# Kernel optimization log

Measured on AMD Instinct MI355X. Metric: run time of the kernel, lower is better.

The kernel has to match this reference:

```python
import jax, jax.numpy as jnp
import numpy as np

B, S, D, H = 4, 2048, 1024, 16
HD = D // H  # head_dim = 64


def setup_inputs() -> dict:
    key = jax.random.key(0)
    kx, kq, kk, kv, ko = jax.random.split(key, 5)
    scale = 1.0 / np.sqrt(D)
    return {
        "x": jax.random.normal(kx, (B, S, D), dtype=jnp.float32),
        "wq": jax.random.normal(kq, (D, D), dtype=jnp.float32) * scale,
        "wk": jax.random.normal(kk, (D, D), dtype=jnp.float32) * scale,
        "wv": jax.random.normal(kv, (D, D), dtype=jnp.float32) * scale,
        "wo": jax.random.normal(ko, (D, D), dtype=jnp.float32) * scale,
    }


def reference(x, wq, wk, wv, wo):
    b, s, d = x.shape
    # nn.Linear stores weight [out, in]: y = x @ W.T
    q = (x @ wq.T).reshape(b, s, H, HD)
    k = (x @ wk.T).reshape(b, s, H, HD)
    v = (x @ wv.T).reshape(b, s, H, HD)
    # scores: [b, h, s, s]
    scores = jnp.einsum("bqhd,bkhd->bhqk", q, k) / np.sqrt(HD)
    causal = jnp.triu(jnp.ones((s, s), dtype=bool), k=1)
    scores = jnp.where(causal, -jnp.inf, scores)
    attn = jax.nn.softmax(scores, axis=-1)
    out = jnp.einsum("bhqk,bkhd->bqhd", attn, v).reshape(b, s, d)
    return out @ wo.T
```

## Files before the change

kernel.cpp:

```cpp
#include <hip/hip_runtime.h>
#include <math.h>

typedef unsigned short u16;
typedef __attribute__((ext_vector_type(8))) short short8;
typedef __attribute__((ext_vector_type(4))) short short4v;
typedef __attribute__((ext_vector_type(4))) float f32x4;

constexpr int Bn = 4, Sn = 2048, Dn = 1024, Hn = 16;
constexpr float SCL = 0.125f * 1.44269504f;

__device__ __forceinline__ u16 f2bf(float f) {
  unsigned u = __float_as_uint(f);
  u += 0x7fffu + ((u >> 16) & 1u);
  return (u16)(u >> 16);
}
__device__ __forceinline__ u16 f2bf_t(float f) {
  return (u16)(__float_as_uint(f) >> 16);
}

__device__ __forceinline__ f32x4 mfma32(short8 a, short8 b, f32x4 c) {
  return __builtin_amdgcn_mfma_f32_16x16x32_bf16(a, b, c, 0, 0, 0);
}

__device__ __forceinline__ f32x4 mfma16(short4v a, short4v b, f32x4 c) {
#if __has_builtin(__builtin_amdgcn_mfma_f32_16x16x16_bf16)
  return __builtin_amdgcn_mfma_f32_16x16x16_bf16(a, b, c, 0, 0, 0);
#elif __has_builtin(__builtin_amdgcn_mfma_f32_16x16x16bf16_1k)
  return __builtin_amdgcn_mfma_f32_16x16x16bf16_1k(a, b, c, 0, 0, 0);
#else
  short8 a8 = {a[0], a[1], a[2], a[3], 0, 0, 0, 0};
  short8 b8 = {b[0], b[1], b[2], b[3], 0, 0, 0, 0};
  return __builtin_amdgcn_mfma_f32_16x16x32_bf16(a8, b8, c, 0, 0, 0);
#endif
}

__device__ __forceinline__ void gl_lds16(const u16* g, u16* l) {
  __builtin_amdgcn_global_load_lds(
      (const __attribute__((address_space(1))) unsigned int*)g,
      (__attribute__((address_space(3))) unsigned int*)l, 16, 0, 0);
}

__global__ __launch_bounds__(256) void cast_x(const float4* __restrict__ in,
                                              ushort4* __restrict__ out, int n4) {
  const int i = blockIdx.x * 256 + threadIdx.x;
  if (i < n4) {
    const float4 f = in[i];
    ushort4 o;
    o.x = f2bf(f.x); o.y = f2bf(f.y); o.z = f2bf(f.z); o.w = f2bf(f.w);
    out[i] = o;
  }
}

__global__ __launch_bounds__(256) void cast_w4(const float4* __restrict__ w0,
                                               const float4* __restrict__ w1,
                                               const float4* __restrict__ w2,
                                               const float4* __restrict__ w3,
                                               ushort4* __restrict__ o0,
                                               ushort4* __restrict__ o1,
                                               ushort4* __restrict__ o2,
                                               ushort4* __restrict__ o3) {
  const int z = blockIdx.y;
  const float4* in = z == 0 ? w0 : z == 1 ? w1 : z == 2 ? w2 : w3;
  ushort4* out = z == 0 ? o0 : z == 1 ? o1 : z == 2 ? o2 : o3;
  const int i = blockIdx.x * 256 + threadIdx.x;
  const float4 f = in[i];
  ushort4 o;
  o.x = f2bf(f.x); o.y = f2bf(f.y); o.z = f2bf(f.z); o.w = f2bf(f.w);
  out[i] = o;
}

template <int MODE>
__device__ __forceinline__ void gemm_body(const u16* __restrict__ A,
                                          const u16* __restrict__ W,
                                          u16* __restrict__ Cb,
                                          float* __restrict__ Cf,
                                          int bx, int by) {
  __shared__ u16 Asm[128 * 32];
  __shared__ u16 Wsm[128 * 32];
  const int t = threadIdx.x;
  const int w = t >> 6, l = t & 63;
  const int wy = w >> 1, wx = w & 1;
  const int q = l >> 4, r = l & 15;
  const int m0 = bx * 128, n0 = by * 128;
  const int c0 = w * 64 + l;

  f32x4 acc[4][4] = {};

  for (int k0 = 0; k0 < 1024; k0 += 32) {
    __syncthreads();
#pragma unroll
    for (int i = 0; i < 2; ++i) {
      const int c = c0 + i * 256;
      const int row = c >> 2, cl = c & 3;
      const int cg = cl ^ ((row >> 1) & 3);
      gl_lds16(A + (size_t)(m0 + row) * 1024 + k0 + cg * 8, &Asm[c * 8]);
      gl_lds16(W + (size_t)(n0 + row) * 1024 + k0 + cg * 8, &Wsm[c * 8]);
    }
    __syncthreads();

    short8 af[4], bf[4];
#pragma unroll
    for (int mi = 0; mi < 4; ++mi) {
      const int rowA = wy * 64 + mi * 16 + r;
      af[mi] = *(const short8*)&Asm[rowA * 32 + (q ^ ((rowA >> 1) & 3)) * 8];
      const int rowB = wx * 64 + mi * 16 + r;
      bf[mi] = *(const short8*)&Wsm[rowB * 32 + (q ^ ((rowB >> 1) & 3)) * 8];
    }
#pragma unroll
    for (int mi = 0; mi < 4; ++mi)
#pragma unroll
      for (int ni = 0; ni < 4; ++ni)
        acc[mi][ni] = mfma32(af[mi], bf[ni], acc[mi][ni]);
  }

  if (MODE == 2) {
    const int bq = m0 >> 11;
    const int jt = ((m0 & 2047) >> 6) + wy;
    const int hh = (n0 >> 6) + wx;
    u16* vt_t = Cb + ((size_t)((bq * 16 + hh) * 32) + jt) * 4096;
#pragma unroll
    for (int mi = 0; mi < 4; ++mi)
#pragma unroll
      for (int ni = 0; ni < 4; ++ni) {
        short4v pk;
#pragma unroll
        for (int e = 0; e < 4; ++e) pk[e] = (short)f2bf(acc[mi][ni][e]);
        const int hd = ni * 16 + r;
        const int c2 = q + 4 * (mi >> 1);
        *(short4v*)&vt_t[hd * 64 + ((c2 ^ (r & 7)) * 8) + (mi & 1) * 4] = pk;
      }
    return;
  }

#pragma unroll
  for (int mi = 0; mi < 4; ++mi) {
    const int row = m0 + wy * 64 + mi * 16 + q * 4;
#pragma unroll
    for (int ni = 0; ni < 4; ++ni) {
      const int col = n0 + wx * 64 + ni * 16 + r;
#pragma unroll
      for (int e = 0; e < 4; ++e) {
        if (MODE == 1)
          Cf[(size_t)(row + e) * 1024 + col] = acc[mi][ni][e];
        else
          Cb[(size_t)(row + e) * 1024 + col] = f2bf(acc[mi][ni][e]);
      }
    }
  }
}

__global__ __launch_bounds__(256) void gemm_qk(const u16* __restrict__ A,
                                               const u16* __restrict__ Wq,
                                               const u16* __restrict__ Wk,
                                               u16* __restrict__ Cq,
                                               u16* __restrict__ Ck) {
  const int z = blockIdx.z;
  gemm_body<0>(A, z ? Wk : Wq, z ? Ck : Cq, nullptr, blockIdx.x, blockIdx.y);
}

__global__ __launch_bounds__(256) void gemm_v(const u16* __restrict__ A,
                                              const u16* __restrict__ W,
                                              u16* __restrict__ Vt) {
  gemm_body<2>(A, W, Vt, nullptr, blockIdx.x, blockIdx.y);
}

__global__ __launch_bounds__(256) void gemm_out(const u16* __restrict__ A,
                                                const u16* __restrict__ W,
                                                float* __restrict__ C) {
  gemm_body<1>(A, W, nullptr, C, blockIdx.x, blockIdx.y);
}

__global__ __launch_bounds__(128) void attn_v5(const u16* __restrict__ Qb,
                                               const u16* __restrict__ Kb,
                                               const u16* __restrict__ Vt,
                                               u16* __restrict__ Ob) {
  const int i = blockIdx.x;
  const int grp = (i & 7) + 8 * (i >> 7);
  const int qp = (i >> 3) & 15;
  const int b = grp >> 4, h = grp & 15;
  const int t = threadIdx.x;
  const int w = t >> 6, l = t & 63;
  const int q = l >> 4, r = l & 15;

  __shared__ u16 Kd[2][4096];
  __shared__ u16 Vd[2][4096];

  const size_t kgbase = (size_t)(b * Sn) * Dn + h * 64;
  const size_t vgbase = (size_t)((b * Hn + h) * 32) * 4096;

#pragma unroll 1
  for (int ph = 0; ph < 2; ++ph) {
    const int st = ph ? 31 - qp : qp;
    const int qb64 = st * 64;

    short8 Qf[2][2];
#pragma unroll
    for (int mi = 0; mi < 2; ++mi)
#pragma unroll
      for (int kf = 0; kf < 2; ++kf)
        Qf[mi][kf] = *(const short8*)(Qb +
            (size_t)(b * Sn + qb64 + w * 32 + mi * 16 + r) * Dn + h * 64 +
            kf * 32 + q * 8);

    f32x4 O[2][4] = {};
    float l_[2] = {0.f, 0.f};

    __syncthreads();
    {
#pragma unroll
      for (int ii = 0; ii < 4; ++ii) {
        const int c = t + ii * 128;
        const int row = c >> 3, cl = c & 7;
        gl_lds16(Kb + kgbase + (size_t)row * Dn + (cl ^ (row & 7)) * 8,
                 &Kd[0][c * 8]);
        gl_lds16(Vt + vgbase + c * 8, &Vd[0][c * 8]);
      }
    }

    for (int jt = 0; jt <= st; ++jt) {
      __syncthreads();
      if (jt < st) {
        const int nb = (jt + 1) & 1;
        const size_t krow0 = kgbase + (size_t)(jt + 1) * 64 * Dn;
        const size_t voff = vgbase + (size_t)(jt + 1) * 4096;
#pragma unroll
        for (int ii = 0; ii < 4; ++ii) {
          const int c = t + ii * 128;
          const int row = c >> 3, cl = c & 7;
          gl_lds16(Kb + krow0 + (size_t)row * Dn + (cl ^ (row & 7)) * 8,
                   &Kd[nb][c * 8]);
          gl_lds16(Vt + voff + c * 8, &Vd[nb][c * 8]);
        }
      }
      const u16* Kt = Kd[jt & 1];
      const u16* Vs = Vd[jt & 1];

      short8 Kf[4][2];
#pragma unroll
      for (int ni = 0; ni < 4; ++ni)
#pragma unroll
        for (int kf = 0; kf < 2; ++kf)
          Kf[ni][kf] =
              *(const short8*)&Kt[(ni * 16 + r) * 64 + ((kf * 4 + q) ^ (r & 7)) * 8];

      f32x4 S[2][4] = {};
#pragma unroll
      for (int ni = 0; ni < 4; ++ni)
#pragma unroll
        for (int kf = 0; kf < 2; ++kf) {
          S[0][ni] = mfma32(Kf[ni][kf], Qf[0][kf], S[0][ni]);
          S[1][ni] = mfma32(Kf[ni][kf], Qf[1][kf], S[1][ni]);
        }

      if (jt == st) {
#pragma unroll
        for (int mi = 0; mi < 2; ++mi) {
          const int qrow = w * 32 + mi * 16 + r;
#pragma unroll
          for (int ni = 0; ni < 4; ++ni) {
            const int key = ni * 16 + q * 4;
#pragma unroll
            for (int e = 0; e < 4; ++e)
              if (key + e > qrow) S[mi][ni][e] = -3.0e38f;
          }
        }
      }

      short4v Pf[2][4];
#pragma unroll
      for (int mi = 0; mi < 2; ++mi)
#pragma unroll
        for (int ni = 0; ni < 4; ++ni) {
          float p0 = __builtin_amdgcn_exp2f(S[mi][ni][0] * SCL);
          float p1 = __builtin_amdgcn_exp2f(S[mi][ni][1] * SCL);
          float p2 = __builtin_amdgcn_exp2f(S[mi][ni][2] * SCL);
          float p3 = __builtin_amdgcn_exp2f(S[mi][ni][3] * SCL);
          l_[mi] += (p0 + p1) + (p2 + p3);
          short4v pf = {(short)f2bf_t(p0), (short)f2bf_t(p1),
                        (short)f2bf_t(p2), (short)f2bf_t(p3)};
          Pf[mi][ni] = pf;
        }

#pragma unroll
      for (int np = 0; np < 2; ++np)
#pragma unroll
        for (int ni2 = 0; ni2 < 4; ++ni2) {
          const short8 vv =
              *(const short8*)&Vs[(ni2 * 16 + r) * 64 + (((q + 4 * np) ^ (r & 7)) * 8)];
          const short4v va = {vv[0], vv[1], vv[2], vv[3]};
          const short4v vb2 = {vv[4], vv[5], vv[6], vv[7]};
          O[0][ni2] = mfma16(va, Pf[0][2 * np], O[0][ni2]);
          O[0][ni2] = mfma16(vb2, Pf[0][2 * np + 1], O[0][ni2]);
          O[1][ni2] = mfma16(va, Pf[1][2 * np], O[1][ni2]);
          O[1][ni2] = mfma16(vb2, Pf[1][2 * np + 1], O[1][ni2]);
        }
    }

#pragma unroll
    for (int mi = 0; mi < 2; ++mi) {
      float s = l_[mi];
      s += __shfl_xor(s, 16, 64);
      s += __shfl_xor(s, 32, 64);
      const float rl = 1.0f / s;
#pragma unroll
      for (int ni2 = 0; ni2 < 4; ++ni2) {
        short4v o;
#pragma unroll
        for (int e = 0; e < 4; ++e) o[e] = (short)f2bf(O[mi][ni2][e] * rl);
        *(short4v*)(Ob + (size_t)(b * Sn + qb64 + w * 32 + mi * 16 + r) * Dn +
                    h * 64 + ni2 * 16 + q * 4) = o;
      }
    }
  }
}

extern "C" void kernel_launch(void* const* d_in, const int* in_sizes, int n_in,
                              void* d_out, int out_size, void* d_ws, size_t ws_size,
                              hipStream_t stream) {
  const float* x  = (const float*)d_in[0];
  const float* wq = (const float*)d_in[1];
  const float* wk = (const float*)d_in[2];
  const float* wv = (const float*)d_in[3];
  const float* wo = (const float*)d_in[4];
  float* out = (float*)d_out;

  u16* xb  = (u16*)d_ws;
  u16* wqb = xb + 8388608;
  u16* wkb = wqb + 1048576;
  u16* wvb = wkb + 1048576;
  u16* wob = wvb + 1048576;
  u16* qb  = wob + 1048576;
  u16* kb  = qb + 8388608;
  u16* vt2 = kb + 8388608;
  u16* aob = vt2 + 8388608;

  cast_x<<<8192, 256, 0, stream>>>((const float4*)x, (ushort4*)xb, 2097152);
  cast_w4<<<dim3(1024, 4), 256, 0, stream>>>(
      (const float4*)wq, (const float4*)wk, (const float4*)wv, (const float4*)wo,
      (ushort4*)wqb, (ushort4*)wkb, (ushort4*)wvb, (ushort4*)wob);

  gemm_qk<<<dim3(64, 8, 2), 256, 0, stream>>>(xb, wqb, wkb, qb, kb);
  gemm_v<<<dim3(64, 8), 256, 0, stream>>>(xb, wvb, vt2);

  attn_v5<<<1024, 128, 0, stream>>>(qb, kb, vt2, aob);

  gemm_out<<<dim3(64, 8), 256, 0, stream>>>(aob, wob, out);
}
```

Measured before the change: 256.8 us.

## Merge cast and QKV launches, fold softmax scale into Wq, tune attention inner loop

Merges the x and weight casts into one launch and the Q/K/V projections into a single three-slice GEMM launch, which removes launch overhead and fills the GPU better. Folds the softmax scale times log2(e) into Wq during the cast, so the per-element multiply before exp2 goes away. In the attention loop it precomputes the global and LDS addresses, raises wave priority around the MFMA blocks, packs probabilities with v_cvt_pk_bf16_f32, and uses a hardware reciprocal. Scaling Wq before rounding to bf16, and rounding rather than truncating P, slightly change the numerics.

```diff
diff --git a/kernel.cpp b/kernel.cpp
--- a/kernel.cpp
+++ b/kernel.cpp
@@ -5,6 +5,7 @@
 typedef __attribute__((ext_vector_type(8))) short short8;
 typedef __attribute__((ext_vector_type(4))) short short4v;
 typedef __attribute__((ext_vector_type(4))) float f32x4;
+typedef __attribute__((ext_vector_type(2))) unsigned int uint2v;
 
 constexpr int Bn = 4, Sn = 2048, Dn = 1024, Hn = 16;
 constexpr float SCL = 0.125f * 1.44269504f;
@@ -13,9 +14,6 @@
   unsigned u = __float_as_uint(f);
   u += 0x7fffu + ((u >> 16) & 1u);
   return (u16)(u >> 16);
-}
-__device__ __forceinline__ u16 f2bf_t(float f) {
-  return (u16)(__float_as_uint(f) >> 16);
 }
 
 __device__ __forceinline__ f32x4 mfma32(short8 a, short8 b, f32x4 c) {
@@ -40,32 +38,33 @@
       (__attribute__((address_space(3))) unsigned int*)l, 16, 0, 0);
 }
 
-__global__ __launch_bounds__(256) void cast_x(const float4* __restrict__ in,
-                                              ushort4* __restrict__ out, int n4) {
-  const int i = blockIdx.x * 256 + threadIdx.x;
-  if (i < n4) {
-    const float4 f = in[i];
-    ushort4 o;
-    o.x = f2bf(f.x); o.y = f2bf(f.y); o.z = f2bf(f.z); o.w = f2bf(f.w);
-    out[i] = o;
-  }
-}
-
-__global__ __launch_bounds__(256) void cast_w4(const float4* __restrict__ w0,
-                                               const float4* __restrict__ w1,
-                                               const float4* __restrict__ w2,
-                                               const float4* __restrict__ w3,
-                                               ushort4* __restrict__ o0,
-                                               ushort4* __restrict__ o1,
-                                               ushort4* __restrict__ o2,
-                                               ushort4* __restrict__ o3) {
-  const int z = blockIdx.y;
-  const float4* in = z == 0 ? w0 : z == 1 ? w1 : z == 2 ? w2 : w3;
-  ushort4* out = z == 0 ? o0 : z == 1 ? o1 : z == 2 ? o2 : o3;
-  const int i = blockIdx.x * 256 + threadIdx.x;
+__global__ __launch_bounds__(256) void cast_all(
+    const float4* __restrict__ x, const float4* __restrict__ wq,
+    const float4* __restrict__ wk, const float4* __restrict__ wv,
+    const float4* __restrict__ wo, ushort4* __restrict__ xb,
+    ushort4* __restrict__ wqb, ushort4* __restrict__ wkb,
+    ushort4* __restrict__ wvb, ushort4* __restrict__ wob) {
+  const int blk = blockIdx.x;
+  const float4* in;
+  ushort4* out;
+  int base;
+  float s = 1.0f;
+  if (blk < 8192) {
+    in = x; out = xb; base = blk;
+  } else if (blk < 9216) {
+    in = wq; out = wqb; base = blk - 8192; s = SCL;
+  } else if (blk < 10240) {
+    in = wk; out = wkb; base = blk - 9216;
+  } else if (blk < 11264) {
+    in = wv; out = wvb; base = blk - 10240;
+  } else {
+    in = wo; out = wob; base = blk - 11264;
+  }
+  const int i = base * 256 + threadIdx.x;
   const float4 f = in[i];
   ushort4 o;
-  o.x = f2bf(f.x); o.y = f2bf(f.y); o.z = f2bf(f.z); o.w = f2bf(f.w);
+  o.x = f2bf(f.x * s); o.y = f2bf(f.y * s);
+  o.z = f2bf(f.z * s); o.w = f2bf(f.w * s);
   out[i] = o;
 }
 
@@ -149,19 +148,18 @@
   }
 }
 
-__global__ __launch_bounds__(256) void gemm_qk(const u16* __restrict__ A,
-                                               const u16* __restrict__ Wq,
-                                               const u16* __restrict__ Wk,
-                                               u16* __restrict__ Cq,
-                                               u16* __restrict__ Ck) {
+__global__ __launch_bounds__(256) void gemm_qkv(const u16* __restrict__ A,
+                                                const u16* __restrict__ Wq,
+                                                const u16* __restrict__ Wk,
+                                                const u16* __restrict__ Wv,
+                                                u16* __restrict__ Cq,
+                                                u16* __restrict__ Ck,
+                                                u16* __restrict__ Vt) {
   const int z = blockIdx.z;
-  gemm_body<0>(A, z ? Wk : Wq, z ? Ck : Cq, nullptr, blockIdx.x, blockIdx.y);
-}
-
-__global__ __launch_bounds__(256) void gemm_v(const u16* __restrict__ A,
-                                              const u16* __restrict__ W,
-                                              u16* __restrict__ Vt) {
-  gemm_body<2>(A, W, Vt, nullptr, blockIdx.x, blockIdx.y);
+  if (z == 2)
+    gemm_body<2>(A, Wv, Vt, nullptr, blockIdx.x, blockIdx.y);
+  else
+    gemm_body<0>(A, z ? Wk : Wq, z ? Ck : Cq, nullptr, blockIdx.x, blockIdx.y);
 }
 
 __global__ __launch_bounds__(256) void gemm_out(const u16* __restrict__ A,
@@ -170,7 +168,7 @@
   gemm_body<1>(A, W, nullptr, C, blockIdx.x, blockIdx.y);
 }
 
-__global__ __launch_bounds__(128) void attn_v5(const u16* __restrict__ Qb,
+__global__ __launch_bounds__(128) void attn_v6(const u16* __restrict__ Qb,
                                                const u16* __restrict__ Kb,
                                                const u16* __restrict__ Vt,
                                                u16* __restrict__ Ob) {
@@ -188,6 +186,18 @@
   const size_t kgbase = (size_t)(b * Sn) * Dn + h * 64;
   const size_t vgbase = (size_t)((b * Hn + h) * 32) * 4096;
 
+  const u16* kg[4];
+  const u16* vg[4];
+#pragma unroll
+  for (int ii = 0; ii < 4; ++ii) {
+    const int c = t + ii * 128, row = c >> 3, cl = c & 7;
+    kg[ii] = Kb + kgbase + (size_t)row * Dn + (cl ^ (row & 7)) * 8;
+    vg[ii] = Vt + vgbase + c * 8;
+  }
+  const int rx = r & 7;
+  const int b0 = r * 64 + ((q ^ rx) * 8);
+  const int b1 = r * 64 + (((4 + q) ^ rx) * 8);
+
 #pragma unroll 1
   for (int ph = 0; ph < 2; ++ph) {
     const int st = ph ? 31 - qp : qp;
@@ -206,44 +216,46 @@
     float l_[2] = {0.f, 0.f};
 
     __syncthreads();
-    {
-#pragma unroll
-      for (int ii = 0; ii < 4; ++ii) {
-        const int c = t + ii * 128;
-        const int row = c >> 3, cl = c & 7;
-        gl_lds16(Kb + kgbase + (size_t)row * Dn + (cl ^ (row & 7)) * 8,
-                 &Kd[0][c * 8]);
-        gl_lds16(Vt + vgbase + c * 8, &Vd[0][c * 8]);
-      }
+#pragma unroll
+    for (int ii = 0; ii < 4; ++ii) {
+      const int c8 = (t + ii * 128) * 8;
+      gl_lds16(kg[ii], &Kd[0][c8]);
+      gl_lds16(vg[ii], &Vd[0][c8]);
+    }
+    const u16* kgt[4];
+    const u16* vgt[4];
+#pragma unroll
+    for (int ii = 0; ii < 4; ++ii) {
+      kgt[ii] = kg[ii] + 64 * Dn;
+      vgt[ii] = vg[ii] + 4096;
     }
 
     for (int jt = 0; jt <= st; ++jt) {
       __syncthreads();
       if (jt < st) {
-        const int nb = (jt + 1) & 1;
-        const size_t krow0 = kgbase + (size_t)(jt + 1) * 64 * Dn;
-        const size_t voff = vgbase + (size_t)(jt + 1) * 4096;
+        u16* kl = &Kd[(jt + 1) & 1][0];
+        u16* vl = &Vd[(jt + 1) & 1][0];
 #pragma unroll
         for (int ii = 0; ii < 4; ++ii) {
-          const int c = t + ii * 128;
-          const int row = c >> 3, cl = c & 7;
-          gl_lds16(Kb + krow0 + (size_t)row * Dn + (cl ^ (row & 7)) * 8,
-                   &Kd[nb][c * 8]);
-          gl_lds16(Vt + voff + c * 8, &Vd[nb][c * 8]);
-        }
-      }
-      const u16* Kt = Kd[jt & 1];
-      const u16* Vs = Vd[jt & 1];
+          const int c8 = (t + ii * 128) * 8;
+          gl_lds16(kgt[ii], kl + c8);
+          gl_lds16(vgt[ii], vl + c8);
+          kgt[ii] += 64 * Dn;
+          vgt[ii] += 4096;
+        }
+      }
+      const u16* KtA = &Kd[jt & 1][b0];
+      const u16* KtB = &Kd[jt & 1][b1];
 
       short8 Kf[4][2];
 #pragma unroll
-      for (int ni = 0; ni < 4; ++ni)
-#pragma unroll
-        for (int kf = 0; kf < 2; ++kf)
-          Kf[ni][kf] =
-              *(const short8*)&Kt[(ni * 16 + r) * 64 + ((kf * 4 + q) ^ (r & 7)) * 8];
+      for (int ni = 0; ni < 4; ++ni) {
+        Kf[ni][0] = *(const short8*)(KtA + ni * 1024);
+        Kf[ni][1] = *(const short8*)(KtB + ni * 1024);
+      }
 
       f32x4 S[2][4] = {};
+      __builtin_amdgcn_s_setprio(1);
 #pragma unroll
       for (int ni = 0; ni < 4; ++ni)
 #pragma unroll
@@ -251,6 +263,7 @@
           S[0][ni] = mfma32(Kf[ni][kf], Qf[0][kf], S[0][ni]);
           S[1][ni] = mfma32(Kf[ni][kf], Qf[1][kf], S[1][ni]);
         }
+      __builtin_amdgcn_s_setprio(0);
 
       if (jt == st) {
 #pragma unroll
@@ -271,22 +284,27 @@
       for (int mi = 0; mi < 2; ++mi)
 #pragma unroll
         for (int ni = 0; ni < 4; ++ni) {
-          float p0 = __builtin_amdgcn_exp2f(S[mi][ni][0] * SCL);
-          float p1 = __builtin_amdgcn_exp2f(S[mi][ni][1] * SCL);
-          float p2 = __builtin_amdgcn_exp2f(S[mi][ni][2] * SCL);
-          float p3 = __builtin_amdgcn_exp2f(S[mi][ni][3] * SCL);
+          const float p0 = __builtin_amdgcn_exp2f(S[mi][ni][0]);
+          const float p1 = __builtin_amdgcn_exp2f(S[mi][ni][1]);
+          const float p2 = __builtin_amdgcn_exp2f(S[mi][ni][2]);
+          const float p3 = __builtin_amdgcn_exp2f(S[mi][ni][3]);
           l_[mi] += (p0 + p1) + (p2 + p3);
-          short4v pf = {(short)f2bf_t(p0), (short)f2bf_t(p1),
-                        (short)f2bf_t(p2), (short)f2bf_t(p3)};
-          Pf[mi][ni] = pf;
-        }
-
+          unsigned plo, phi;
+          asm("v_cvt_pk_bf16_f32 %0, %1, %2" : "=v"(plo) : "v"(p0), "v"(p1));
+          asm("v_cvt_pk_bf16_f32 %0, %1, %2" : "=v"(phi) : "v"(p2), "v"(p3));
+          const uint2v pk2 = {plo, phi};
+          Pf[mi][ni] = __builtin_bit_cast(short4v, pk2);
+        }
+
+      const u16* VsA = &Vd[jt & 1][b0];
+      const u16* VsB = &Vd[jt & 1][b1];
+      __builtin_amdgcn_s_setprio(1);
 #pragma unroll
       for (int np = 0; np < 2; ++np)
 #pragma unroll
         for (int ni2 = 0; ni2 < 4; ++ni2) {
           const short8 vv =
-              *(const short8*)&Vs[(ni2 * 16 + r) * 64 + (((q + 4 * np) ^ (r & 7)) * 8)];
+              *(const short8*)((np ? VsB : VsA) + ni2 * 1024);
           const short4v va = {vv[0], vv[1], vv[2], vv[3]};
           const short4v vb2 = {vv[4], vv[5], vv[6], vv[7]};
           O[0][ni2] = mfma16(va, Pf[0][2 * np], O[0][ni2]);
@@ -294,6 +312,7 @@
           O[1][ni2] = mfma16(va, Pf[1][2 * np], O[1][ni2]);
           O[1][ni2] = mfma16(vb2, Pf[1][2 * np + 1], O[1][ni2]);
         }
+      __builtin_amdgcn_s_setprio(0);
     }
 
 #pragma unroll
@@ -301,7 +320,7 @@
       float s = l_[mi];
       s += __shfl_xor(s, 16, 64);
       s += __shfl_xor(s, 32, 64);
-      const float rl = 1.0f / s;
+      const float rl = __builtin_amdgcn_rcpf(s);
 #pragma unroll
       for (int ni2 = 0; ni2 < 4; ++ni2) {
         short4v o;
@@ -334,15 +353,14 @@
   u16* vt2 = kb + 8388608;
   u16* aob = vt2 + 8388608;
 
-  cast_x<<<8192, 256, 0, stream>>>((const float4*)x, (ushort4*)xb, 2097152);
-  cast_w4<<<dim3(1024, 4), 256, 0, stream>>>(
-      (const float4*)wq, (const float4*)wk, (const float4*)wv, (const float4*)wo,
-      (ushort4*)wqb, (ushort4*)wkb, (ushort4*)wvb, (ushort4*)wob);
-
-  gemm_qk<<<dim3(64, 8, 2), 256, 0, stream>>>(xb, wqb, wkb, qb, kb);
-  gemm_v<<<dim3(64, 8), 256, 0, stream>>>(xb, wvb, vt2);
-
-  attn_v5<<<1024, 128, 0, stream>>>(qb, kb, vt2, aob);
+  cast_all<<<12288, 256, 0, stream>>>(
+      (const float4*)x, (const float4*)wq, (const float4*)wk,
+      (const float4*)wv, (const float4*)wo, (ushort4*)xb, (ushort4*)wqb,
+      (ushort4*)wkb, (ushort4*)wvb, (ushort4*)wob);
+
+  gemm_qkv<<<dim3(64, 8, 3), 256, 0, stream>>>(xb, wqb, wkb, wvb, qb, kb, vt2);
+
+  attn_v6<<<1024, 128, 0, stream>>>(qb, kb, vt2, aob);
 
   gemm_out<<<dim3(64, 8), 256, 0, stream>>>(aob, wob, out);
 }
```

Result: faster. 240.8 us (-6.2%).
